# Performance work log

Measured on AMD Instinct MI355X. Metric: run time of the kernel, lower is better.

The kernel has to match this reference:

```python
import jax, jax.numpy as jnp
import numpy as np

THRESHOLD = 0.8
EPS = 1e-9


def setup_inputs() -> dict:
    key = jax.random.key(0)
    k1, k2, k3 = jax.random.split(key, 3)
    B, N = 8, 4096
    # valid boxes: x1<x2, y1<y2, inside unit image
    xy = jax.random.uniform(k1, (B, N, 2), dtype=jnp.float32) * 0.5
    wh = jax.random.uniform(k2, (B, N, 2), dtype=jnp.float32) * 0.5 + 1e-3
    boxes = jnp.concatenate([xy, xy + wh], axis=-1)  # [B,N,4] = x1,y1,x2,y2
    class_ids = jax.random.randint(k3, (B, N), 0, 80, dtype=jnp.int32)
    return {"boxes": boxes, "class_ids": class_ids}


def reference(boxes, class_ids):
    """Filter large boxes whose same-class fully-contained boxes cover > threshold of their area.

    boxes: [B,N,4] float32 (x1,y1,x2,y2); class_ids: [B,N] int32.
    Returns (masked_boxes [B,N,4], keep_mask [B,N]).
    Note: the original sorts by area descending before the pairwise compare, but the
    per-box contained-area sum and keep decision are permutation-invariant, so the
    sort is skipped here (identical keep set on original indices).
    """
    x1, y1, x2, y2 = boxes[..., 0], boxes[..., 1], boxes[..., 2], boxes[..., 3]
    areas = (x2 - x1) * (y2 - y1)  # [B,N]
    # contained[b,i,j] = True iff box j is fully inside box i
    contained = (
        (x1[:, None, :] >= x1[:, :, None])
        & (y1[:, None, :] >= y1[:, :, None])
        & (x2[:, None, :] <= x2[:, :, None])
        & (y2[:, None, :] <= y2[:, :, None])
    )  # [B,N,N]
    same_class = class_ids[:, :, None] == class_ids[:, None, :]  # [B,N,N]
    N = boxes.shape[1]
    not_diag = ~jnp.eye(N, dtype=bool)[None]  # exclude self-containment
    valid = contained & same_class & not_diag
    # sum of areas of all (other, same-class) boxes contained in box i
    sum_contained = jnp.sum(jnp.where(valid, areas[:, None, :], jnp.float32(0.0)), axis=-1)
    keep = sum_contained <= THRESHOLD * (areas + EPS)  # [B,N]
    return boxes * keep[..., None].astype(boxes.dtype), keep
```

## Files before the change

kernel.cpp:

```cpp
#include <hip/hip_runtime.h>

#define BATCH 8
#define NBOX 4096
#define NCLS 80
#define THRESH 0.8f
#define EPSV 1e-9f
#define WAVES 4
#define TPB (WAVES * 64)
#define PERW (NBOX / WAVES)
#define WITER (PERW / 64)
#define WCAP 96
#define LCAP (WAVES * WCAP)

__global__ __launch_bounds__(TPB) void class_filter_kernel(
    const float* __restrict__ boxes,
    const int* __restrict__ cls,
    float* __restrict__ out)
{
    __shared__ int    segIdx[LCAP];
    __shared__ int    wcnt[WAVES];
    __shared__ float4 lbox[LCAP];
    __shared__ float2 lai[LCAP];

    const int b = blockIdx.x / NCLS;
    const int c = blockIdx.x % NCLS;
    const int tid  = threadIdx.x;
    const int w    = tid >> 6;
    const int lane = tid & 63;
    const int w0   = w * PERW;

    const float4* bx = reinterpret_cast<const float4*>(boxes) + (size_t)b * NBOX;
    const int* cl = cls + (size_t)b * NBOX;

    int myc[WITER];
#pragma unroll
    for (int it = 0; it < WITER; ++it) myc[it] = cl[w0 + it * 64 + lane];

    int run = 0;
#pragma unroll
    for (int it = 0; it < WITER; ++it) {
        const bool m = (myc[it] == c);
        const unsigned long long mask = __ballot(m);
        const int pos = run + (int)__popcll(mask & ((1ull << lane) - 1ull));
        if (m && pos < WCAP) segIdx[w * WCAP + pos] = w0 + it * 64 + lane;
        run += (int)__popcll(mask);
    }
    if (lane == 0) wcnt[w] = run;
    __syncthreads();

    int psum[WAVES + 1];
    psum[0] = 0;
    bool ovf = false;
#pragma unroll
    for (int ww = 0; ww < WAVES; ++ww) {
        int v = wcnt[ww];
        ovf |= (v > WCAP);
        psum[ww + 1] = psum[ww] + v;
    }
    const int len = psum[WAVES];

    float*  keepOut = out + (size_t)BATCH * NBOX * 4;
    float4* boxOut  = reinterpret_cast<float4*>(out);

    if (!ovf) {
        if (tid < len) {
            int wsel = 0;
#pragma unroll
            for (int ww = 1; ww < WAVES; ++ww) if (tid >= psum[ww]) wsel = ww;
            const int idx = segIdx[wsel * WCAP + (tid - psum[wsel])];
            float4 bb = bx[idx];
            lbox[tid] = bb;
            lai[tid]  = make_float2((bb.z - bb.x) * (bb.w - bb.y),
                                    __int_as_float(idx));
        }
        __syncthreads();

        if (tid < len) {
            const float4 bi = lbox[tid];
            const int mi = __float_as_int(lai[tid].y);
            float sum = 0.f;
            for (int k = 0; k < len; ++k) {
                float4 bj = lbox[k];
                float2 aj = lai[k];
                float m = fmaxf(fmaxf(bi.x - bj.x, bi.y - bj.y),
                                fmaxf(bj.z - bi.z, bj.w - bi.w));
                bool cont = (m <= 0.f) && (__float_as_int(aj.y) != mi);
                sum += cont ? aj.x : 0.f;
            }
            const float area = lai[tid].x;
            const float kf = (sum <= THRESH * (area + EPSV)) ? 1.f : 0.f;
            const int g = b * NBOX + mi;
            boxOut[g] = make_float4(bi.x * kf, bi.y * kf, bi.z * kf, bi.w * kf);
            keepOut[g] = kf;
        }
    } else {
        for (int i0 = 0; i0 < NBOX; i0 += TPB) {
            const int i = i0 + tid;
            if (cl[i] != c) continue;
            float4 bi = bx[i];
            float area = (bi.z - bi.x) * (bi.w - bi.y);
            float sum = 0.f;
            for (int j = 0; j < NBOX; ++j) {
                if (cl[j] != c || j == i) continue;
                float4 bj = bx[j];
                float m = fmaxf(fmaxf(bi.x - bj.x, bi.y - bj.y),
                                fmaxf(bj.z - bi.z, bj.w - bi.w));
                sum += (m <= 0.f) ? (bj.z - bj.x) * (bj.w - bj.y) : 0.f;
            }
            float kf = (sum <= THRESH * (area + EPSV)) ? 1.f : 0.f;
            const int g = b * NBOX + i;
            boxOut[g] = make_float4(bi.x * kf, bi.y * kf, bi.z * kf, bi.w * kf);
            keepOut[g] = kf;
        }
    }
}

extern "C" void kernel_launch(void* const* d_in, const int* in_sizes, int n_in,
                              void* d_out, int out_size, void* d_ws, size_t ws_size,
                              hipStream_t stream) {
    const float* boxes = (const float*)d_in[0];
    const int*   cls   = (const int*)d_in[1];
    float* out = (float*)d_out;

    class_filter_kernel<<<BATCH * NCLS, TPB, 0, stream>>>(boxes, cls, out);
}
```

Baseline: 59.89 us.

## Process five classes per block to amortize class-id scan and fill threads

Each block now handles five classes instead of one, so the grid shrinks from 640 to 128 blocks. The class-id array is read once per block and ballot-compacted for all five classes. All 256 threads then work on the combined compacted list rather than only the ~51 that matched a single class. The aim is to cut redundant reads of the class array and idle lanes. The risks are fewer blocks than compute units on the GPU, more serial prefix work on thread 0, and a larger chance of falling into the slow overflow path because the per-wave cap dropped to 48.

Measured after the change: 65.24 us. 8.9% more time.

```diff
diff --git a/kernel.cpp b/kernel.cpp
--- a/kernel.cpp
+++ b/kernel.cpp
@@ -9,25 +9,32 @@
 #define TPB (WAVES * 64)
 #define PERW (NBOX / WAVES)
 #define WITER (PERW / 64)
-#define WCAP 96
-#define LCAP (WAVES * WCAP)
+#define NCPB 5
+#define CBLK (NCLS / NCPB)
+#define WCAP 48
+#define CCAP 128
 
 __global__ __launch_bounds__(TPB) void class_filter_kernel(
     const float* __restrict__ boxes,
     const int* __restrict__ cls,
     float* __restrict__ out)
 {
-    __shared__ int    segIdx[LCAP];
-    __shared__ int    wcnt[WAVES];
-    __shared__ float4 lbox[LCAP];
-    __shared__ float2 lai[LCAP];
+    __shared__ int    segIdx[NCPB][WAVES][WCAP];
+    __shared__ int    wcnt[NCPB][WAVES];
+    __shared__ int    sPs[NCPB][WAVES + 1];
+    __shared__ int    sCum[NCPB + 1];
+    __shared__ int    sLen[NCPB];
+    __shared__ int    sOvf;
+    __shared__ float4 lbox[NCPB * CCAP];
+    __shared__ float2 lai[NCPB * CCAP];
 
-    const int b = blockIdx.x / NCLS;
-    const int c = blockIdx.x % NCLS;
+    const int b  = blockIdx.x / CBLK;
+    const int c0 = (blockIdx.x % CBLK) * NCPB;
     const int tid  = threadIdx.x;
     const int w    = tid >> 6;
     const int lane = tid & 63;
     const int w0   = w * PERW;
+    const unsigned long long lmask = (1ull << lane) - 1ull;
 
     const float4* bx = reinterpret_cast<const float4*>(boxes) + (size_t)b * NBOX;
     const int* cl = cls + (size_t)b * NBOX;
@@ -36,81 +43,134 @@
 #pragma unroll
     for (int it = 0; it < WITER; ++it) myc[it] = cl[w0 + it * 64 + lane];
 
-    int run = 0;
+    int run0 = 0, run1 = 0, run2 = 0, run3 = 0, run4 = 0;
 #pragma unroll
     for (int it = 0; it < WITER; ++it) {
-        const bool m = (myc[it] == c);
-        const unsigned long long mask = __ballot(m);
-        const int pos = run + (int)__popcll(mask & ((1ull << lane) - 1ull));
-        if (m && pos < WCAP) segIdx[w * WCAP + pos] = w0 + it * 64 + lane;
-        run += (int)__popcll(mask);
+        const int idx = w0 + it * 64 + lane;
+        {
+            unsigned long long m = __ballot(myc[it] == c0 + 0);
+            int p = run0 + (int)__popcll(m & lmask);
+            if ((myc[it] == c0 + 0) && p < WCAP) segIdx[0][w][p] = idx;
+            run0 += (int)__popcll(m);
+        }
+        {
+            unsigned long long m = __ballot(myc[it] == c0 + 1);
+            int p = run1 + (int)__popcll(m & lmask);
+            if ((myc[it] == c0 + 1) && p < WCAP) segIdx[1][w][p] = idx;
+            run1 += (int)__popcll(m);
+        }
+        {
+            unsigned long long m = __ballot(myc[it] == c0 + 2);
+            int p = run2 + (int)__popcll(m & lmask);
+            if ((myc[it] == c0 + 2) && p < WCAP) segIdx[2][w][p] = idx;
+            run2 += (int)__popcll(m);
+        }
+        {
+            unsigned long long m = __ballot(myc[it] == c0 + 3);
+            int p = run3 + (int)__popcll(m & lmask);
+            if ((myc[it] == c0 + 3) && p < WCAP) segIdx[3][w][p] = idx;
+            run3 += (int)__popcll(m);
+        }
+        {
+            unsigned long long m = __ballot(myc[it] == c0 + 4);
+            int p = run4 + (int)__popcll(m & lmask);
+            if ((myc[it] == c0 + 4) && p < WCAP) segIdx[4][w][p] = idx;
+            run4 += (int)__popcll(m);
+        }
     }
-    if (lane == 0) wcnt[w] = run;
+    if (lane == 0) {
+        wcnt[0][w] = run0; wcnt[1][w] = run1; wcnt[2][w] = run2;
+        wcnt[3][w] = run3; wcnt[4][w] = run4;
+    }
     __syncthreads();
 
-    int psum[WAVES + 1];
-    psum[0] = 0;
-    bool ovf = false;
-#pragma unroll
-    for (int ww = 0; ww < WAVES; ++ww) {
-        int v = wcnt[ww];
-        ovf |= (v > WCAP);
-        psum[ww + 1] = psum[ww] + v;
+    if (tid == 0) {
+        int cum = 0, ovf = 0;
+        for (int cc = 0; cc < NCPB; ++cc) {
+            int p = 0;
+            sPs[cc][0] = 0;
+            for (int ww = 0; ww < WAVES; ++ww) {
+                int v = wcnt[cc][ww];
+                if (v > WCAP) ovf = 1;
+                p += v;
+                sPs[cc][ww + 1] = p;
+            }
+            sLen[cc] = p;
+            if (p > CCAP) ovf = 1;
+            sCum[cc] = cum;
+            cum += p;
+        }
+        sCum[NCPB] = cum;
+        sOvf = ovf;
     }
-    const int len = psum[WAVES];
+    __syncthreads();
 
     float*  keepOut = out + (size_t)BATCH * NBOX * 4;
     float4* boxOut  = reinterpret_cast<float4*>(out);
 
-    if (!ovf) {
-        if (tid < len) {
+    if (!sOvf) {
+        const int tot = sCum[NCPB];
+
+        for (int t = tid; t < tot; t += TPB) {
+            int cc = 0;
+#pragma unroll
+            for (int q = 1; q < NCPB; ++q) if (t >= sCum[q]) cc = q;
+            const int r = t - sCum[cc];
             int wsel = 0;
 #pragma unroll
-            for (int ww = 1; ww < WAVES; ++ww) if (tid >= psum[ww]) wsel = ww;
-            const int idx = segIdx[wsel * WCAP + (tid - psum[wsel])];
+            for (int ww = 1; ww < WAVES; ++ww) if (r >= sPs[cc][ww]) wsel = ww;
+            const int idx = segIdx[cc][wsel][r - sPs[cc][wsel]];
             float4 bb = bx[idx];
-            lbox[tid] = bb;
-            lai[tid]  = make_float2((bb.z - bb.x) * (bb.w - bb.y),
-                                    __int_as_float(idx));
+            lbox[cc * CCAP + r] = bb;
+            lai[cc * CCAP + r] = make_float2((bb.z - bb.x) * (bb.w - bb.y),
+                                             __int_as_float(idx));
         }
         __syncthreads();
 
-        if (tid < len) {
-            const float4 bi = lbox[tid];
-            const int mi = __float_as_int(lai[tid].y);
+        for (int t = tid; t < tot; t += TPB) {
+            int cc = 0;
+#pragma unroll
+            for (int q = 1; q < NCPB; ++q) if (t >= sCum[q]) cc = q;
+            const int r = t - sCum[cc];
+            const float4 bi = lbox[cc * CCAP + r];
+            const int mi = __float_as_int(lai[cc * CCAP + r].y);
+            const int n = sLen[cc];
             float sum = 0.f;
-            for (int k = 0; k < len; ++k) {
-                float4 bj = lbox[k];
-                float2 aj = lai[k];
+            for (int k = 0; k < n; ++k) {
+                float4 bj = lbox[cc * CCAP + k];
+                float2 aj = lai[cc * CCAP + k];
                 float m = fmaxf(fmaxf(bi.x - bj.x, bi.y - bj.y),
                                 fmaxf(bj.z - bi.z, bj.w - bi.w));
                 bool cont = (m <= 0.f) && (__float_as_int(aj.y) != mi);
                 sum += cont ? aj.x : 0.f;
             }
-            const float area = lai[tid].x;
+            const float area = lai[cc * CCAP + r].x;
             const float kf = (sum <= THRESH * (area + EPSV)) ? 1.f : 0.f;
             const int g = b * NBOX + mi;
             boxOut[g] = make_float4(bi.x * kf, bi.y * kf, bi.z * kf, bi.w * kf);
             keepOut[g] = kf;
         }
     } else {
-        for (int i0 = 0; i0 < NBOX; i0 += TPB) {
-            const int i = i0 + tid;
-            if (cl[i] != c) continue;
-            float4 bi = bx[i];
-            float area = (bi.z - bi.x) * (bi.w - bi.y);
-            float sum = 0.f;
-            for (int j = 0; j < NBOX; ++j) {
-                if (cl[j] != c || j == i) continue;
-                float4 bj = bx[j];
-                float m = fmaxf(fmaxf(bi.x - bj.x, bi.y - bj.y),
-                                fmaxf(bj.z - bi.z, bj.w - bi.w));
-                sum += (m <= 0.f) ? (bj.z - bj.x) * (bj.w - bj.y) : 0.f;
+        for (int cc = 0; cc < NCPB; ++cc) {
+            const int c = c0 + cc;
+            for (int i0 = 0; i0 < NBOX; i0 += TPB) {
+                const int i = i0 + tid;
+                if (cl[i] != c) continue;
+                float4 bi = bx[i];
+                float area = (bi.z - bi.x) * (bi.w - bi.y);
+                float sum = 0.f;
+                for (int j = 0; j < NBOX; ++j) {
+                    if (cl[j] != c || j == i) continue;
+                    float4 bj = bx[j];
+                    float m = fmaxf(fmaxf(bi.x - bj.x, bi.y - bj.y),
+                                    fmaxf(bj.z - bi.z, bj.w - bi.w));
+                    sum += (m <= 0.f) ? (bj.z - bj.x) * (bj.w - bj.y) : 0.f;
+                }
+                float kf = (sum <= THRESH * (area + EPSV)) ? 1.f : 0.f;
+                const int g = b * NBOX + i;
+                boxOut[g] = make_float4(bi.x * kf, bi.y * kf, bi.z * kf, bi.w * kf);
+                keepOut[g] = kf;
             }
-            float kf = (sum <= THRESH * (area + EPSV)) ? 1.f : 0.f;
-            const int g = b * NBOX + i;
-            boxOut[g] = make_float4(bi.x * kf, bi.y * kf, bi.z * kf, bi.w * kf);
-            keepOut[g] = kf;
         }
     }
 }
@@ -122,5 +182,5 @@
     const int*   cls   = (const int*)d_in[1];
     float* out = (float*)d_out;
 
-    class_filter_kernel<<<BATCH * NCLS, TPB, 0, stream>>>(boxes, cls, out);
+    class_filter_kernel<<<BATCH * CBLK, TPB, 0, stream>>>(boxes, cls, out);
 }
```
